# Kernel optimization log

Measured on AMD Instinct MI355X. Metric: run time of the kernel, lower is better.

## Reference

```python
import jax, jax.numpy as jnp
import numpy as np

B, H, W, CIN = 8, 32, 32, 64
COUT, NOUT, KH, KW = 64, 32, 3, 3


def setup_inputs() -> dict:
    key = jax.random.key(0)
    ks = jax.random.split(key, 7)
    n_flat = H * W * COUT  # conv output flattened (same padding, stride 1)
    return {
        "x": jax.random.normal(ks[0], (B, H, W, CIN), jnp.float32),
        "w_out_u": jax.random.normal(ks[1], (B, 1, n_flat, NOUT), jnp.float32) * 0.05,
        "b_out_u": jax.random.normal(ks[2], (B, 1, NOUT), jnp.float32),
        "w_out_l": jax.random.normal(ks[3], (B, 1, n_flat, NOUT), jnp.float32) * 0.05,
        "b_out_l": jax.random.normal(ks[4], (B, 1, NOUT), jnp.float32),
        "kernel": jax.random.normal(ks[5], (KH, KW, CIN, COUT), jnp.float32) * 0.1,
        "bias": jax.random.normal(ks[6], (COUT,), jnp.float32),
    }


def reference(x, w_out_u, b_out_u, w_out_l, b_out_l, kernel, bias):
    Bb, Hh, Ww, Cin = x.shape
    Cout = kernel.shape[-1]
    n_out = w_out_u.shape[-1]
    # 'same' padding, stride 1 -> conv output spatial dims equal input dims
    Ho, Wo = Hh, Ww

    # [B,1,n_flat,n_out] -> [B,n_out,Ho,Wo,Cout]
    wu = jnp.transpose(w_out_u, (0, 1, 3, 2)).reshape(Bb, n_out, Ho, Wo, Cout)
    wl = jnp.transpose(w_out_l, (0, 1, 3, 2)).reshape(Bb, n_out, Ho, Wo, Cout)

    # bias contribution: sum over spatial + channel -> [B, n_out] -> [B,1,n_out]
    b_u = jnp.sum(wu * bias, axis=(2, 3, 4))[:, None, :] + b_out_u
    b_l = jnp.sum(wl * bias, axis=(2, 3, 4))[:, None, :] + b_out_l

    # conv2d_transpose(z, kernel) == adjoint (vjp) of the forward conv.
    # Batch the per-n_out transposed convs (the K.rnn loop) into one call.
    def conv_fwd(z):  # z: [N,H,W,Cin] -> [N,Ho,Wo,Cout]
        return jax.lax.conv_general_dilated(
            z, kernel, window_strides=(1, 1), padding="SAME",
            dimension_numbers=("NHWC", "HWIO", "NHWC"))

    zeros_in = jnp.zeros((Bb * n_out, Hh, Ww, Cin), wu.dtype)
    _, vjp_fn = jax.vjp(conv_fwd, zeros_in)

    def conv_t(w):  # [B,n_out,Ho,Wo,Cout] -> [B,n_out,H,W,Cin]
        g = vjp_fn(w.reshape(Bb * n_out, Ho, Wo, Cout))[0]
        return g.reshape(Bb, n_out, Hh, Ww, Cin)

    wu_t = conv_t(wu)
    wl_t = conv_t(wl)

    n_in = Hh * Ww * Cin
    w_u_out = jnp.transpose(wu_t.reshape(Bb, 1, n_out, n_in), (0, 1, 3, 2))
    w_l_out = jnp.transpose(wl_t.reshape(Bb, 1, n_out, n_in), (0, 1, 3, 2))
    return (w_u_out, b_u, w_l_out, b_l)
```

## Files before the change

### kernel.cpp

```cpp
#include <hip/hip_runtime.h>
#include <cstdint>

typedef __attribute__((ext_vector_type(8))) short short8;
typedef __attribute__((ext_vector_type(16))) float f32x16;
typedef __attribute__((ext_vector_type(4))) unsigned int uint4v;

__device__ inline uint32_t f2bf(float f) {
    union { float f; uint32_t u; } x; x.f = f;
    return (x.u + 0x7FFF + ((x.u >> 16) & 1)) >> 16;
}
__device__ inline uint32_t fbits(float f) {
    union { float f; uint32_t u; } x; x.f = f;
    return x.u;
}
__device__ inline float bflo(uint32_t u) {
    union { uint32_t u; float f; } x; x.u = u << 16; return x.f;
}
__device__ inline float bfhi(uint32_t u) {
    union { uint32_t u; float f; } x; x.u = u & 0xFFFF0000u; return x.f;
}

__device__ inline void dma16(const void* g, void* lds) {
    __builtin_amdgcn_global_load_lds(
        (const __attribute__((address_space(1))) unsigned int*)g,
        (__attribute__((address_space(3))) unsigned int*)lds, 16, 0, 0);
}

__global__ __launch_bounds__(256) void k_xform(
    const float* __restrict__ wu, const float* __restrict__ wl,
    uint4v* __restrict__ X,
    const float* __restrict__ kk, uint4v* __restrict__ AF,
    const float* __restrict__ buI, const float* __restrict__ blI,
    float* __restrict__ buO, float* __restrict__ blO)
{
    int tid = blockIdx.x * 256 + threadIdx.x;

    if (tid < 512 + 4608) {
        if (tid < 256) buO[tid] = buI[tid];
        else if (tid < 512) blO[tid - 256] = blI[tid - 256];
        else {
            int a    = tid - 512;
            int al   = a & 63;
            int c    = (a >> 6) & 1;
            int kidx = (a >> 7) & 3;
            int tap  = a >> 9;
            const float* kp = kk + ((size_t)tap * 64 + c * 32 + (al & 31)) * 64
                                 + kidx * 16 + (al >> 5) * 8;
            uint4v w;
            #pragma unroll
            for (int pr = 0; pr < 4; pr++)
                w[pr] = f2bf(kp[2 * pr]) | (f2bf(kp[2 * pr + 1]) << 16);
            AF[((tap * 4 + kidx) * 2 + c) * 64 + al] = w;
        }
    }

    int l    = tid & 63;
    int kidx = (tid >> 6) & 3;
    int site = (tid >> 8) & 1023;
    int img  = tid >> 18;
    int b    = img >> 1;
    const float* src = (img & 1) ? wl : wu;
    int o = l & 31, ch = l >> 5;

    const float* p = src + ((size_t)b * 65536 + (size_t)site * 64
                            + kidx * 16 + ch * 8) * 32 + o;
    uint4v w;
    #pragma unroll
    for (int pr = 0; pr < 4; pr++) {
        float g0 = p[(2 * pr) * 32];
        float g1 = p[(2 * pr + 1) * 32];
        w[pr] = __builtin_amdgcn_perm(fbits(g1), fbits(g0), 0x07060302u);
    }
    X[tid] = w;
}

__global__ __launch_bounds__(256, 4) void k_conv(
    const uint16_t* __restrict__ X, const uint16_t* __restrict__ AF,
    const float* __restrict__ bias,
    float* __restrict__ outU, float* __restrict__ outL,
    float* __restrict__ buO, float* __restrict__ blO)
{
    __shared__ uint16_t tiles[6][4][512];

    int tdx  = threadIdx.x;
    int l    = tdx & 63;
    int wid  = tdx >> 6;
    int o    = l & 31;
    int ch   = l >> 5;
    int c    = wid >> 1;
    int wsel = wid & 1;

    int bid = blockIdx.x;
    int b   = bid & 7;
    int v   = bid >> 3;
    int h   = v & 31;
    int wq  = v >> 5;
    int w0  = wq * 4 + wsel * 2;

    int rstart = (h == 31) ? 1 : 0;
    int nr     = (h == 0 || h == 31) ? 2 : 3;

    const char* XB  = (const char*)X;
    const char* AFB = (const char*)AF;

    for (int UL = 0; UL < 2; UL++) {
        int img = b * 2 + UL;
        float* dst  = UL ? outL : outU;
        float* bdst = UL ? blO : buO;

        float bp = 0.f;
        f32x16 acc[2];
        acc[0] = (f32x16)0.f;
        acc[1] = (f32x16)0.f;

        for (int i = 0; i < nr; i++) {
            int r  = rstart + i;
            int hh = h + 1 - r;

            __syncthreads();

            #pragma unroll
            for (int p = 0; p < 6; p++) {
                int pc = wid * 6 + p;
                int s = pc >> 2, k = pc & 3;
                int ww = wq * 4 - 1 + s;
                void* ldst = (void*)&tiles[s][k][0];
                if ((unsigned)ww < 32u) {
                    const char* g = XB + ((size_t)(img * 1024 + hh * 32 + ww)) * 4096
                                       + (size_t)k * 1024 + (size_t)l * 16;
                    dma16(g, ldst);
                } else {
                    *(uint4v*)((char*)ldst + l * 16) = (uint4v)0u;
                }
            }

            __syncthreads();

            __builtin_amdgcn_s_setprio(1);
            #pragma unroll
            for (int kidx = 0; kidx < 4; kidx++) {
                short8 A[3];
                #pragma unroll
                for (int kw = 0; kw < 3; kw++)
                    A[kw] = *(const short8*)(AFB
                            + (size_t)((((r * 3 + kw) * 4 + kidx) * 2 + c) * 64 + l) * 16);

                uint4v bw[4];
                #pragma unroll
                for (int si = 0; si < 4; si++) {
                    int s = 2 * wsel + si;
                    bw[si] = *(const uint4v*)((const char*)&tiles[s][kidx][0] + l * 16);
                }

                if (r == 1 && c == 0) {
                    float4 b0 = *(const float4*)(bias + kidx * 16 + ch * 8);
                    float4 b1 = *(const float4*)(bias + kidx * 16 + ch * 8 + 4);
                    float bb[8] = {b0.x, b0.y, b0.z, b0.w, b1.x, b1.y, b1.z, b1.w};
                    #pragma unroll
                    for (int pr = 0; pr < 4; pr++) {
                        bp = fmaf(bflo(bw[1][pr]), bb[2 * pr],
                             fmaf(bfhi(bw[1][pr]), bb[2 * pr + 1], bp));
                        bp = fmaf(bflo(bw[2][pr]), bb[2 * pr],
                             fmaf(bfhi(bw[2][pr]), bb[2 * pr + 1], bp));
                    }
                }

                #pragma unroll
                for (int si = 0; si < 4; si++) {
                    short8 Bf = __builtin_bit_cast(short8, bw[si]);
                    #pragma unroll
                    for (int tw = 0; tw < 2; tw++) {
                        int kw = tw + 2 - si;
                        if (kw >= 0 && kw <= 2)
                            acc[tw] = __builtin_amdgcn_mfma_f32_32x32x16_bf16(
                                A[kw], Bf, acc[tw], 0, 0, 0);
                    }
                }
            }
            __builtin_amdgcn_s_setprio(0);
        }

        bp += __shfl_xor(bp, 32);
        if (l < 32 && c == 0) atomicAdd(&bdst[b * 32 + o], bp);

        #pragma unroll
        for (int tw = 0; tw < 2; tw++) {
            int w = w0 + tw;
            float* base = dst + ((size_t)b * 65536 + (size_t)(h * 32 + w) * 64 + c * 32) * 32;
            #pragma unroll
            for (int reg = 0; reg < 16; reg++) {
                int row = (reg & 3) + 8 * (reg >> 2) + 4 * (l >> 5);
                base[row * 32 + o] = acc[tw][reg];
            }
        }
    }
}

extern "C" void kernel_launch(void* const* d_in, const int* in_sizes, int n_in,
                              void* d_out, int out_size, void* d_ws, size_t ws_size,
                              hipStream_t stream) {
    const float* wu   = (const float*)d_in[1];
    const float* buI  = (const float*)d_in[2];
    const float* wl   = (const float*)d_in[3];
    const float* blI  = (const float*)d_in[4];
    const float* kk   = (const float*)d_in[5];
    const float* bias = (const float*)d_in[6];

    float* out  = (float*)d_out;
    float* outU = out;
    float* buO  = out + 16777216;
    float* outL = out + 16777216 + 256;
    float* blO  = out + 2 * 16777216 + 256;

    uint4v* AF = (uint4v*)d_ws;
    const size_t XOFF = 131072;
    uint4v* X = (uint4v*)((char*)d_ws + XOFF);

    k_xform<<<16384, 256, 0, stream>>>(wu, wl, X, kk, AF, buI, blI, buO, blO);
    k_conv<<<2048, 256, 0, stream>>>((const uint16_t*)X, (const uint16_t*)AF, bias,
                                     outU, outL, buO, blO);
}
```

Baseline: 108.4 us.

## Process 8 output rows per block with a rolling 3-row LDS ring buffer

Each conv block now handles one image (U or L) and a strip of 8 output rows, instead of one row for both images. Input rows are staged into a 3-slot ring buffer in LDS, so each row is loaded once and reused across the three kernel-row taps, not reloaded up to three times. The next row is prefetched while outputs are stored. Grid size falls from 2048 to 512 blocks and the occupancy hint drops from 4 to 2, which reduces parallelism and adds more barriers per block in exchange for less redundant global traffic.

```diff
diff --git a/kernel.cpp b/kernel.cpp
--- a/kernel.cpp
+++ b/kernel.cpp
@@ -74,13 +74,13 @@
     X[tid] = w;
 }
 
-__global__ __launch_bounds__(256, 4) void k_conv(
+__global__ __launch_bounds__(256, 2) void k_conv(
     const uint16_t* __restrict__ X, const uint16_t* __restrict__ AF,
     const float* __restrict__ bias,
     float* __restrict__ outU, float* __restrict__ outL,
     float* __restrict__ buO, float* __restrict__ blO)
 {
-    __shared__ uint16_t tiles[6][4][512];
+    __shared__ uint16_t tiles[3][6][4][512];
 
     int tdx  = threadIdx.x;
     int l    = tdx & 63;
@@ -93,50 +93,57 @@
     int bid = blockIdx.x;
     int b   = bid & 7;
     int v   = bid >> 3;
-    int h   = v & 31;
-    int wq  = v >> 5;
+    int hs  = v & 3;
+    int wq  = (v >> 2) & 7;
+    int UL  = v >> 5;
+    int h0  = hs * 8;
     int w0  = wq * 4 + wsel * 2;
-
-    int rstart = (h == 31) ? 1 : 0;
-    int nr     = (h == 0 || h == 31) ? 2 : 3;
+    int img = b * 2 + UL;
+
+    float* dst  = UL ? outL : outU;
+    float* bdst = UL ? blO : buO;
 
     const char* XB  = (const char*)X;
     const char* AFB = (const char*)AF;
 
-    for (int UL = 0; UL < 2; UL++) {
-        int img = b * 2 + UL;
-        float* dst  = UL ? outL : outU;
-        float* bdst = UL ? blO : buO;
-
-        float bp = 0.f;
+    float bp = 0.f;
+
+    auto STAGE = [&](int hh) {
+        int sl = (hh + 3) % 3;
+        bool rowv = (unsigned)hh < 32u;
+        #pragma unroll
+        for (int p = 0; p < 6; p++) {
+            int pc = wid * 6 + p;
+            int s = pc >> 2, k = pc & 3;
+            int ww = wq * 4 - 1 + s;
+            void* ldst = (void*)&tiles[sl][s][k][0];
+            if (rowv && (unsigned)ww < 32u) {
+                const char* g = XB + ((size_t)(img * 1024 + hh * 32 + ww)) * 4096
+                                   + (size_t)k * 1024 + (size_t)l * 16;
+                dma16(g, ldst);
+            } else {
+                *(uint4v*)((char*)ldst + l * 16) = (uint4v)0u;
+            }
+        }
+    };
+
+    STAGE(h0 - 1);
+    STAGE(h0);
+    STAGE(h0 + 1);
+    __syncthreads();
+
+    for (int i = 0; i < 8; i++) {
+        int h = h0 + i;
+
         f32x16 acc[2];
         acc[0] = (f32x16)0.f;
         acc[1] = (f32x16)0.f;
 
-        for (int i = 0; i < nr; i++) {
-            int r  = rstart + i;
-            int hh = h + 1 - r;
-
-            __syncthreads();
-
-            #pragma unroll
-            for (int p = 0; p < 6; p++) {
-                int pc = wid * 6 + p;
-                int s = pc >> 2, k = pc & 3;
-                int ww = wq * 4 - 1 + s;
-                void* ldst = (void*)&tiles[s][k][0];
-                if ((unsigned)ww < 32u) {
-                    const char* g = XB + ((size_t)(img * 1024 + hh * 32 + ww)) * 4096
-                                       + (size_t)k * 1024 + (size_t)l * 16;
-                    dma16(g, ldst);
-                } else {
-                    *(uint4v*)((char*)ldst + l * 16) = (uint4v)0u;
-                }
-            }
-
-            __syncthreads();
-
-            __builtin_amdgcn_s_setprio(1);
+        #pragma unroll
+        for (int wr = 0; wr < 3; wr++) {
+            int hh = h - 1 + wr;
+            int r  = 2 - wr;
+            int sl = (hh + 3) % 3;
             #pragma unroll
             for (int kidx = 0; kidx < 4; kidx++) {
                 short8 A[3];
@@ -149,7 +156,7 @@
                 #pragma unroll
                 for (int si = 0; si < 4; si++) {
                     int s = 2 * wsel + si;
-                    bw[si] = *(const uint4v*)((const char*)&tiles[s][kidx][0] + l * 16);
+                    bw[si] = *(const uint4v*)((const char*)&tiles[sl][s][kidx][0] + l * 16);
                 }
 
                 if (r == 1 && c == 0) {
@@ -177,11 +184,11 @@
                     }
                 }
             }
-            __builtin_amdgcn_s_setprio(0);
-        }
-
-        bp += __shfl_xor(bp, 32);
-        if (l < 32 && c == 0) atomicAdd(&bdst[b * 32 + o], bp);
+        }
+
+        __syncthreads();
+
+        if (i < 7) STAGE(h + 2);
 
         #pragma unroll
         for (int tw = 0; tw < 2; tw++) {
@@ -193,7 +200,12 @@
                 base[row * 32 + o] = acc[tw][reg];
             }
         }
+
+        __syncthreads();
     }
+
+    bp += __shfl_xor(bp, 32);
+    if (l < 32 && c == 0) atomicAdd(&bdst[b * 32 + o], bp);
 }
 
 extern "C" void kernel_launch(void* const* d_in, const int* in_sizes, int n_in,
@@ -217,6 +229,6 @@
     uint4v* X = (uint4v*)((char*)d_ws + XOFF);
 
     k_xform<<<16384, 256, 0, stream>>>(wu, wl, X, kk, AF, buI, blI, buO, blO);
-    k_conv<<<2048, 256, 0, stream>>>((const uint16_t*)X, (const uint16_t*)AF, bias,
-                                     outU, outL, buO, blO);
-}
+    k_conv<<<512, 256, 0, stream>>>((const uint16_t*)X, (const uint16_t*)AF, bias,
+                                    outU, outL, buO, blO);
+}
```

Result: faster. 102.6 us (-5.3%).
